# Performance work log

Measured on AMD Instinct MI355X. Metric: run time of the kernel, lower is better.

Reference implementation:

```python
import jax, jax.numpy as jnp
import numpy as np

N_NODES = 50000
N_EDGES = 800000
IN_F = 256
HID = 128
OUT_F = 128
HEADS = 4
NEG_SLOPE = 0.2


def setup_inputs() -> dict:
    key = jax.random.key(0)
    ks = jax.random.split(key, 10)
    x = jax.random.normal(ks[0], (N_NODES, IN_F), dtype=jnp.float32)
    edge_index = jax.random.randint(ks[1], (2, N_EDGES), 0, N_NODES, dtype=jnp.int64)
    # layer 1: in=256 -> heads=4, ch=128
    W1 = jax.random.normal(ks[2], (HEADS * HID, IN_F), dtype=jnp.float32) / np.sqrt(IN_F)
    att_src1 = jax.random.normal(ks[3], (HEADS, HID), dtype=jnp.float32) / np.sqrt(HID)
    att_dst1 = jax.random.normal(ks[4], (HEADS, HID), dtype=jnp.float32) / np.sqrt(HID)
    b1 = jnp.zeros((HID,), dtype=jnp.float32)
    # layer 2: in=128 -> heads=4, ch=128
    W2 = jax.random.normal(ks[5], (HEADS * OUT_F, HID), dtype=jnp.float32) / np.sqrt(HID)
    att_src2 = jax.random.normal(ks[6], (HEADS, OUT_F), dtype=jnp.float32) / np.sqrt(OUT_F)
    att_dst2 = jax.random.normal(ks[7], (HEADS, OUT_F), dtype=jnp.float32) / np.sqrt(OUT_F)
    b2 = jnp.zeros((OUT_F,), dtype=jnp.float32)
    return {"x": x, "edge_index": edge_index,
            "W1": W1, "att_src1": att_src1, "att_dst1": att_dst1, "b1": b1,
            "W2": W2, "att_src2": att_src2, "att_dst2": att_dst2, "b2": b2}


def gat_conv(x, src, dst, W, att_src, att_dst, b, heads, ch):
    n = x.shape[0]
    xh = (x @ W.T).reshape(n, heads, ch)                 # [N,H,C]
    a_s = jnp.einsum('nhc,hc->nh', xh, att_src)          # [N,H]
    a_d = jnp.einsum('nhc,hc->nh', xh, att_dst)
    alpha = a_s[src] + a_d[dst]                          # [E,H]
    alpha = jnp.where(alpha >= 0, alpha, NEG_SLOPE * alpha)
    # segment softmax over destination nodes
    amax = jax.ops.segment_max(alpha, dst, num_segments=n)
    amax = jnp.where(jnp.isfinite(amax), amax, 0.0)
    e = jnp.exp(alpha - amax[dst])                       # [E,H]
    denom = jax.ops.segment_sum(e, dst, num_segments=n)  # [N,H]
    coef = e / (denom[dst] + 1e-16)                      # [E,H]
    msg = xh[src] * coef[:, :, None]                     # [E,H,C]
    out = jax.ops.segment_sum(msg, dst, num_segments=n)  # [N,H,C]
    return out.mean(axis=1) + b                          # concat=False -> mean over heads


def reference(x, edge_index, W1, att_src1, att_dst1, b1, W2, att_src2, att_dst2, b2):
    n = x.shape[0]
    loops = jnp.arange(n, dtype=edge_index.dtype)
    src = jnp.concatenate([edge_index[0], loops])        # add_self_loops=True (PyG default)
    dst = jnp.concatenate([edge_index[1], loops])
    h = gat_conv(x, src, dst, W1, att_src1, att_dst1, b1, HEADS, HID)
    return gat_conv(h, src, dst, W2, att_src2, att_dst2, b2, HEADS, OUT_F)
```

## Files before the change

kernel.cpp:

```cpp
#include <hip/hip_runtime.h>
#include <hip/hip_fp16.h>
#include <math.h>

#define N_NODES 50000
#define MPAD    50176
#define N_EDGES 800000
#define E_TOT   (N_EDGES + N_NODES)
#define EB      ((E_TOT + 255) / 256)
#define HEADS   4
#define NEG_SLOPE 0.2f
#define SBLK    ((N_NODES + 255) / 256)

typedef unsigned int u32;
typedef unsigned short u16;
typedef __attribute__((ext_vector_type(8))) _Float16 f16x8;
typedef __attribute__((ext_vector_type(4))) float f32x4;



__global__ __launch_bounds__(256) void prep(const int* __restrict__ ei,
                                            int* __restrict__ deg,
                                            const float* __restrict__ W1,
                                            __half* __restrict__ B1,
                                            const float* __restrict__ W2,
                                            __half* __restrict__ B2,
                                            const float* __restrict__ att_s1,
                                            const float* __restrict__ att_d1,
                                            const float* __restrict__ att_s2,
                                            const float* __restrict__ att_d2,
                                            float* __restrict__ ws1,
                                            float* __restrict__ wd1,
                                            float* __restrict__ ws2,
                                            float* __restrict__ wd2) {
  int b = blockIdx.x, tid = threadIdx.x;
  if (b < EB) {
    int e = b * 256 + tid;
    if (e < E_TOT) {
      int dst = (e < N_EDGES) ? ei[N_EDGES + e] : (e - N_EDGES);
      atomicAdd(&deg[dst], 1);
    }
    return;
  }
  if (b < EB + 128) {
    int k4 = (b - EB) * 256 + tid;
    float4 v = ((const float4*)W1)[k4];
    __half2 h01 = __float22half2_rn(make_float2(v.x, v.y));
    __half2 h23 = __float22half2_rn(make_float2(v.z, v.w));
    uint2 pk = make_uint2(*(u32*)&h01, *(u32*)&h23);
    int r = k4 >> 6, h = r >> 7, j = r & 127;
    ((uint2*)B1)[j * 256 + h * 64 + (k4 & 63)] = pk;
    return;
  }
  if (b < EB + 192) {
    int k4 = (b - EB - 128) * 256 + tid;
    float4 v = ((const float4*)W2)[k4];
    __half2 h01 = __float22half2_rn(make_float2(v.x, v.y));
    __half2 h23 = __float22half2_rn(make_float2(v.z, v.w));
    uint2 pk = make_uint2(*(u32*)&h01, *(u32*)&h23);
    int r = k4 >> 5, h = r >> 7, j = r & 127;
    ((uint2*)B2)[j * 128 + h * 32 + (k4 & 31)] = pk;
    return;
  }
  int bw = b - (EB + 192);
  int h = bw & 3;
  if (bw < 8) {
    const float* att = (bw < 4) ? att_s1 : att_d1;
    float* o = (bw < 4) ? ws1 : wd1;
    int k = tid;
    float acc = 0.f;
    for (int c = 0; c < 128; ++c)
      acc = fmaf(att[h * 128 + c], W1[(size_t)(h * 128 + c) * 256 + k], acc);
    o[h * 256 + k] = acc;
  } else {
    const float* att = (bw < 12) ? att_s2 : att_d2;
    float* o = (bw < 12) ? ws2 : wd2;
    if (tid < 128) {
      int k = tid;
      float acc = 0.f;
      for (int c = 0; c < 128; ++c)
        acc = fmaf(att[h * 128 + c], W2[(size_t)(h * 128 + c) * 128 + k], acc);
      o[h * 128 + k] = acc;
    }
  }
}


__global__ __launch_bounds__(256) void scan_blocks(const int* __restrict__ deg,
                                                   int* __restrict__ row_ptr,
                                                   int* __restrict__ bsum) {
  __shared__ int sh[256];
  int tid = threadIdx.x;
  int idx = blockIdx.x * 256 + tid;
  int v = (idx < N_NODES) ? deg[idx] : 0;
  sh[tid] = v;
  __syncthreads();
#pragma unroll
  for (int off = 1; off < 256; off <<= 1) {
    int t = (tid >= off) ? sh[tid - off] : 0;
    __syncthreads();
    sh[tid] += t;
    __syncthreads();
  }
  if (idx < N_NODES) row_ptr[idx + 1] = sh[tid];
  if (tid == 255) bsum[blockIdx.x] = sh[255];
}

__global__ __launch_bounds__(256) void scan_tops(int* __restrict__ bsum) {
  __shared__ int sh[256];
  int tid = threadIdx.x;
  int v = (tid < SBLK) ? bsum[tid] : 0;
  sh[tid] = v;
  __syncthreads();
#pragma unroll
  for (int off = 1; off < 256; off <<= 1) {
    int t = (tid >= off) ? sh[tid - off] : 0;
    __syncthreads();
    sh[tid] += t;
    __syncthreads();
  }
  if (tid < SBLK) bsum[tid] = sh[tid] - v;
}

__global__ __launch_bounds__(256) void scan_add(const int* __restrict__ bsum,
                                                int* __restrict__ row_ptr) {
  int idx = blockIdx.x * 256 + threadIdx.x;
  int off = bsum[blockIdx.x];
  if (idx < N_NODES) row_ptr[idx + 1] += off;
  if (idx == 0) row_ptr[0] = 0;
}

__device__ __forceinline__ float leaky_exp(float a) {
  a = (a >= 0.f) ? a : NEG_SLOPE * a;
  return __expf(a);
}

__global__ __launch_bounds__(256) void scatter_edges_w(const int* __restrict__ ei,
                                                       const int* __restrict__ row_ptr,
                                                       int* __restrict__ cursor,
                                                       const float* __restrict__ as_,
                                                       const float* __restrict__ ad_,
                                                       int* __restrict__ col,
                                                       int* __restrict__ dstarr,
                                                       float4* __restrict__ wtab) {
  int e = blockIdx.x * 256 + threadIdx.x;
  if (e >= E_TOT) return;
  int src, dst;
  if (e < N_EDGES) { src = ei[e]; dst = ei[N_EDGES + e]; }
  else             { src = e - N_EDGES; dst = src; }
  int pos = atomicAdd(&cursor[dst], 1);
  int slot = row_ptr[dst] + pos;
  col[slot] = src;
  dstarr[slot] = dst;
  float4 a = ((const float4*)as_)[src];
  float4 d = ((const float4*)ad_)[dst];
  float4 w;
  w.x = leaky_exp(a.x + d.x);
  w.y = leaky_exp(a.y + d.y);
  w.z = leaky_exp(a.z + d.z);
  w.w = leaky_exp(a.w + d.w);
  wtab[slot] = w;
}

__global__ __launch_bounds__(256) void edge_weights2(const int* __restrict__ col,
                                                     const int* __restrict__ dstarr,
                                                     const float* __restrict__ as_,
                                                     const float* __restrict__ ad_,
                                                     float4* __restrict__ wtab) {
  int i = blockIdx.x * 256 + threadIdx.x;
  if (i >= E_TOT) return;
  int src = col[i], dst = dstarr[i];
  float4 a = ((const float4*)as_)[src];
  float4 d = ((const float4*)ad_)[dst];
  float4 w;
  w.x = leaky_exp(a.x + d.x);
  w.y = leaky_exp(a.y + d.y);
  w.z = leaky_exp(a.z + d.z);
  w.w = leaky_exp(a.w + d.w);
  wtab[i] = w;
}


__global__ __launch_bounds__(256) void prep_x(const float* __restrict__ x,
                                              const float* __restrict__ ws1,
                                              const float* __restrict__ wd1,
                                              __half* __restrict__ x16,
                                              float* __restrict__ as_,
                                              float* __restrict__ ad_) {
  int node = (blockIdx.x * 256 + threadIdx.x) >> 6;
  if (node >= N_NODES) return;
  int lane = threadIdx.x & 63;
  int c4 = lane * 4;
  f32x4 xv = *(const f32x4*)(x + (size_t)node * 256 + c4);
  __half2 h01 = __float22half2_rn(make_float2(xv[0], xv[1]));
  __half2 h23 = __float22half2_rn(make_float2(xv[2], xv[3]));
  uint2 pk = make_uint2(*(u32*)&h01, *(u32*)&h23);
  *(uint2*)(x16 + (size_t)node * 256 + c4) = pk;
  float p[8];
#pragma unroll
  for (int v = 0; v < 4; ++v) {
    f32x4 w = *(const f32x4*)(ws1 + v * 256 + c4);
    p[v] = xv[0] * w[0] + xv[1] * w[1] + xv[2] * w[2] + xv[3] * w[3];
    f32x4 u = *(const f32x4*)(wd1 + v * 256 + c4);
    p[4 + v] = xv[0] * u[0] + xv[1] * u[1] + xv[2] * u[2] + xv[3] * u[3];
  }
#pragma unroll
  for (int k = 0; k < 8; ++k)
#pragma unroll
    for (int m = 1; m < 64; m <<= 1)
      p[k] += __shfl_xor(p[k], m, 64);
  if (lane == 0) {
    *(float4*)(as_ + (size_t)node * 4) = make_float4(p[0], p[1], p[2], p[3]);
    *(float4*)(ad_ + (size_t)node * 4) = make_float4(p[4], p[5], p[6], p[7]);
  }
}


__global__ __launch_bounds__(256) void score2(const __half* __restrict__ hrow,
                                              const float* __restrict__ ws2,
                                              const float* __restrict__ wd2,
                                              float* __restrict__ as_,
                                              float* __restrict__ ad_) {
  int node = (blockIdx.x * 256 + threadIdx.x) >> 6;
  if (node >= N_NODES) return;
  int lane = threadIdx.x & 63, c = lane * 2;
  float2 f = __half22float2(*(const __half2*)(hrow + (size_t)node * 128 + c));
  float p[8];
#pragma unroll
  for (int v = 0; v < 4; ++v) {
    float2 w = *(const float2*)(ws2 + v * 128 + c);
    p[v] = f.x * w.x + f.y * w.y;
    float2 u = *(const float2*)(wd2 + v * 128 + c);
    p[4 + v] = f.x * u.x + f.y * u.y;
  }
#pragma unroll
  for (int k = 0; k < 8; ++k)
#pragma unroll
    for (int m = 1; m < 64; m <<= 1)
      p[k] += __shfl_xor(p[k], m, 64);
  if (lane == 0) {
    *(float4*)(as_ + (size_t)node * 4) = make_float4(p[0], p[1], p[2], p[3]);
    *(float4*)(ad_ + (size_t)node * 4) = make_float4(p[4], p[5], p[6], p[7]);
  }
}


template <int CPL>
__global__ __launch_bounds__(256) void gat_aggregate_w(
    const __half* __restrict__ tbl, const float4* __restrict__ wtab,
    const int* __restrict__ row_ptr, const int* __restrict__ col,
    __half* __restrict__ agg) {
  constexpr int CHIN = CPL * 64;
  int node = (blockIdx.x * 256 + threadIdx.x) >> 6;
  if (node >= N_NODES) return;
  int lane = threadIdx.x & 63, cb = lane * CPL;
  const __half* tb = tbl + cb;
  int s = __builtin_amdgcn_readfirstlane(row_ptr[node]);
  int e = __builtin_amdgcn_readfirstlane(row_ptr[node + 1]);

  float acc[4][CPL];
#pragma unroll
  for (int h = 0; h < 4; ++h)
#pragma unroll
    for (int c = 0; c < CPL; ++c) acc[h][c] = 0.f;
  float den[4] = {0.f, 0.f, 0.f, 0.f};

  auto accum = [&](uint2 q, float4 w) {
    float wv[4] = {w.x, w.y, w.z, w.w};
#pragma unroll
    for (int h = 0; h < 4; ++h) den[h] += wv[h];
    float f[CPL];
    float2 f0 = __half22float2(*(__half2*)&q.x);
    f[0] = f0.x; f[1] = f0.y;
    if (CPL == 4) {
      float2 f1 = __half22float2(*(__half2*)&q.y);
      f[2] = f1.x; f[3] = f1.y;
    }
#pragma unroll
    for (int h = 0; h < 4; ++h)
#pragma unroll
      for (int c = 0; c < CPL; ++c)
        acc[h][c] = fmaf(wv[h], f[c], acc[h][c]);
  };
  auto loadq = [&](int src) -> uint2 {
    if (CPL == 4) return *(const uint2*)(tb + (size_t)src * CHIN);
    uint2 r; r.x = *(const u32*)(tb + (size_t)src * CHIN); r.y = 0;
    return r;
  };

  int i = s;
  for (; i + 4 <= e; i += 4) {
    int s0 = __builtin_amdgcn_readfirstlane(col[i]);
    int s1 = __builtin_amdgcn_readfirstlane(col[i + 1]);
    int s2 = __builtin_amdgcn_readfirstlane(col[i + 2]);
    int s3 = __builtin_amdgcn_readfirstlane(col[i + 3]);
    float4 w0 = wtab[i],     w1 = wtab[i + 1];
    float4 w2 = wtab[i + 2], w3 = wtab[i + 3];
    uint2 q0 = loadq(s0), q1 = loadq(s1), q2 = loadq(s2), q3 = loadq(s3);
    accum(q0, w0); accum(q1, w1); accum(q2, w2); accum(q3, w3);
  }
  for (; i < e; ++i) {
    int s0 = __builtin_amdgcn_readfirstlane(col[i]);
    float4 w0 = wtab[i];
    accum(loadq(s0), w0);
  }

#pragma unroll
  for (int h = 0; h < 4; ++h) {
    float inv = 1.f / (den[h] + 1e-16f);
    if (CPL == 4) {
      __half2 o0 = __float22half2_rn(make_float2(acc[h][0] * inv, acc[h][1] * inv));
      __half2 o1 = __float22half2_rn(make_float2(acc[h][2] * inv, acc[h][3] * inv));
      *(uint2*)(agg + (size_t)node * 4 * CHIN + h * CHIN + cb) =
          make_uint2(*(u32*)&o0, *(u32*)&o1);
    } else {
      __half2 o0 = __float22half2_rn(make_float2(acc[h][0] * inv, acc[h][1] * inv));
      *(u32*)(agg + (size_t)node * 4 * CHIN + h * CHIN + cb) = *(u32*)&o0;
    }
  }
}


#define GLD16(gp, lp)                                                          \
  __builtin_amdgcn_global_load_lds(                                            \
      (const __attribute__((address_space(1))) u32*)(gp),                      \
      (__attribute__((address_space(3))) u32*)(lp), 16, 0, 0)

template <int K, bool HALF_OUT>
__global__ __launch_bounds__(512, 4) void gemm_mean(
    const __half* __restrict__ A, const __half* __restrict__ Bm,
    const float* __restrict__ bias, void* __restrict__ outv) {
  __shared__ u16 sA[256 * 32];
  __shared__ u16 sB[128 * 32];
  const int tid = threadIdx.x, lane = tid & 63, wave = tid >> 6;
  const int m0 = blockIdx.x * 256;
  const int wm = (wave >> 1) * 64, wn = (wave & 1) * 64;
  const int t = lane & 15, quad = lane >> 4;

  f32x4 acc[4][4];
#pragma unroll
  for (int i = 0; i < 4; i++)
#pragma unroll
    for (int j = 0; j < 4; j++) acc[i][j] = (f32x4){0.f, 0.f, 0.f, 0.f};

  const char* gpA[2]; u32 offA[2];
#pragma unroll
  for (int r = 0; r < 2; ++r) {
    int c = tid + r * 512;
    int row = c >> 2, w16 = c & 3;
    gpA[r] = (const char*)A + ((size_t)(m0 + row) * K) * 2 + w16 * 16;
    offA[r] = (u32)c * 16;
  }
  const char* gpB;
  {
    int row = tid >> 2, w16 = tid & 3;
    gpB = (const char*)Bm + ((size_t)row * K) * 2 + w16 * 16;
  }
  u32 offB = (u32)tid * 16;

  for (int k0 = 0; k0 < K; k0 += 32) {
    __syncthreads();
#pragma unroll
    for (int r = 0; r < 2; ++r) { GLD16(gpA[r], (char*)sA + offA[r]); gpA[r] += 64; }
    GLD16(gpB, (char*)sB + offB); gpB += 64;
    __syncthreads();

    f16x8 a[4], b[4];
#pragma unroll
    for (int i = 0; i < 4; ++i) {
      a[i] = *(const f16x8*)&sA[(wm + t + i * 16) * 32 + quad * 8];
      b[i] = *(const f16x8*)&sB[(wn + t + i * 16) * 32 + quad * 8];
    }
#pragma unroll
    for (int i = 0; i < 4; ++i)
#pragma unroll
      for (int j = 0; j < 4; ++j)
        acc[i][j] = __builtin_amdgcn_mfma_f32_16x16x32_f16(a[i], b[j], acc[i][j], 0, 0, 0);
  }

  float bv[4];
#pragma unroll
  for (int j = 0; j < 4; ++j) bv[j] = bias[wn + j * 16 + t];
#pragma unroll
  for (int i = 0; i < 4; ++i)
#pragma unroll
    for (int j = 0; j < 4; ++j)
#pragma unroll
      for (int r = 0; r < 4; ++r) {
        int m = m0 + wm + i * 16 + quad * 4 + r;
        if (m < N_NODES) {
          int n = wn + j * 16 + t;
          float v = 0.25f * acc[i][j][r] + bv[j];
          if (HALF_OUT) ((__half*)outv)[(size_t)m * 128 + n] = __float2half(v);
          else          ((float*)outv)[(size_t)m * 128 + n] = v;
        }
      }
}


extern "C" void kernel_launch(void* const* d_in, const int* in_sizes, int n_in,
                              void* d_out, int out_size, void* d_ws, size_t ws_size,
                              hipStream_t stream) {
  const float* x      = (const float*)d_in[0];
  const int*   ei     = (const int*)  d_in[1];
  const float* W1     = (const float*)d_in[2];
  const float* att_s1 = (const float*)d_in[3];
  const float* att_d1 = (const float*)d_in[4];
  const float* b1     = (const float*)d_in[5];
  const float* W2     = (const float*)d_in[6];
  const float* att_s2 = (const float*)d_in[7];
  const float* att_d2 = (const float*)d_in[8];
  const float* b2     = (const float*)d_in[9];
  float* out = (float*)d_out;

  char* ws = (char*)d_ws;
  size_t off = 0;
  auto alloc = [&](size_t bytes) -> void* {
    void* p = ws + off;
    off += (bytes + 255) & ~(size_t)255;
    return p;
  };
  __half* x16  = (__half*)alloc((size_t)MPAD * 256 * 2);
  __half* agg1 = (__half*)alloc((size_t)MPAD * 1024 * 2);
  __half* B1p  = (__half*)alloc((size_t)128 * 1024 * 2);
  __half* B2p  = (__half*)alloc((size_t)128 * 512 * 2);
  float* ws1 = (float*)alloc(4 * 256 * 4);
  float* wd1 = (float*)alloc(4 * 256 * 4);
  float* ws2 = (float*)alloc(4 * 128 * 4);
  float* wd2 = (float*)alloc(4 * 128 * 4);
  float* as1 = (float*)alloc((size_t)N_NODES * 4 * 4);
  float* ad1 = (float*)alloc((size_t)N_NODES * 4 * 4);
  float* as2 = (float*)alloc((size_t)N_NODES * 4 * 4);
  float* ad2 = (float*)alloc((size_t)N_NODES * 4 * 4);
  int*   row_ptr = (int*)alloc((size_t)(N_NODES + 1) * 4);
  int*   deg     = (int*)alloc((size_t)N_NODES * 4);
  int*   cursor  = (int*)alloc((size_t)N_NODES * 4);
  int*   bsum    = (int*)alloc((size_t)256 * 4);
  int*   col     = (int*)alloc((size_t)E_TOT * 4);
  int*   dstarr  = (int*)alloc((size_t)E_TOT * 4);
  float4* wtab   = (float4*)alloc((size_t)E_TOT * 16);

  __half* out1 = x16;
  __half* agg2 = agg1;

  const int edge_blocks = (E_TOT + 255) / 256;
  const int node_wave_blocks = (N_NODES + 3) / 4;

  hipMemsetAsync(deg, 0, (size_t)N_NODES * 2 * 4 + 256, stream);
  prep<<<EB + 208, 256, 0, stream>>>(ei, deg, W1, B1p, W2, B2p,
                                     att_s1, att_d1, att_s2, att_d2,
                                     ws1, wd1, ws2, wd2);
  scan_blocks<<<SBLK, 256, 0, stream>>>(deg, row_ptr, bsum);
  scan_tops<<<1, 256, 0, stream>>>(bsum);
  scan_add<<<SBLK, 256, 0, stream>>>(bsum, row_ptr);

  prep_x<<<node_wave_blocks, 256, 0, stream>>>(x, ws1, wd1, x16, as1, ad1);
  scatter_edges_w<<<edge_blocks, 256, 0, stream>>>(ei, row_ptr, cursor,
                                                   as1, ad1, col, dstarr, wtab);
  gat_aggregate_w<4><<<node_wave_blocks, 256, 0, stream>>>(
      x16, wtab, row_ptr, col, agg1);
  gemm_mean<1024, true><<<MPAD / 256, 512, 0, stream>>>(agg1, B1p, b1, out1);

  score2<<<node_wave_blocks, 256, 0, stream>>>(out1, ws2, wd2, as2, ad2);
  edge_weights2<<<edge_blocks, 256, 0, stream>>>(col, dstarr, as2, ad2, wtab);
  gat_aggregate_w<2><<<node_wave_blocks, 256, 0, stream>>>(
      out1, wtab, row_ptr, col, agg2);
  gemm_mean<512, false><<<MPAD / 256, 512, 0, stream>>>(agg2, B2p, b2, out);
}
```

Measured before the change: 440.1 us.

## Record edge slot positions during degree count and pack src/dst pairs

The degree-counting atomic now stores each edge's returned position, so the CSR scatter no longer needs a second cursor atomic pass. Source and destination are packed into one int2 array, replacing separate col and dst arrays, and a single edge_weights kernel serves both layers. The layer-1 edge-weight computation now runs as its own kernel reading the packed array, which adds a launch and an extra pass over the edges. The aggregate kernels read source indices at stride 2 from the packed array, which halves the useful bytes per cache line.

```diff
diff --git a/kernel.cpp b/kernel.cpp
--- a/kernel.cpp
+++ b/kernel.cpp
@@ -20,6 +20,7 @@
 
 __global__ __launch_bounds__(256) void prep(const int* __restrict__ ei,
                                             int* __restrict__ deg,
+                                            int* __restrict__ epos,
                                             const float* __restrict__ W1,
                                             __half* __restrict__ B1,
                                             const float* __restrict__ W2,
@@ -37,7 +38,7 @@
     int e = b * 256 + tid;
     if (e < E_TOT) {
       int dst = (e < N_EDGES) ? ei[N_EDGES + e] : (e - N_EDGES);
-      atomicAdd(&deg[dst], 1);
+      epos[e] = atomicAdd(&deg[dst], 1);
     }
     return;
   }
@@ -134,43 +135,30 @@
   return __expf(a);
 }
 
-__global__ __launch_bounds__(256) void scatter_edges_w(const int* __restrict__ ei,
-                                                       const int* __restrict__ row_ptr,
-                                                       int* __restrict__ cursor,
-                                                       const float* __restrict__ as_,
-                                                       const float* __restrict__ ad_,
-                                                       int* __restrict__ col,
-                                                       int* __restrict__ dstarr,
-                                                       float4* __restrict__ wtab) {
+
+__global__ __launch_bounds__(256) void scatter_pos(const int* __restrict__ ei,
+                                                   const int* __restrict__ epos,
+                                                   const int* __restrict__ row_ptr,
+                                                   int2* __restrict__ col2) {
   int e = blockIdx.x * 256 + threadIdx.x;
   if (e >= E_TOT) return;
   int src, dst;
   if (e < N_EDGES) { src = ei[e]; dst = ei[N_EDGES + e]; }
   else             { src = e - N_EDGES; dst = src; }
-  int pos = atomicAdd(&cursor[dst], 1);
-  int slot = row_ptr[dst] + pos;
-  col[slot] = src;
-  dstarr[slot] = dst;
-  float4 a = ((const float4*)as_)[src];
-  float4 d = ((const float4*)ad_)[dst];
-  float4 w;
-  w.x = leaky_exp(a.x + d.x);
-  w.y = leaky_exp(a.y + d.y);
-  w.z = leaky_exp(a.z + d.z);
-  w.w = leaky_exp(a.w + d.w);
-  wtab[slot] = w;
-}
-
-__global__ __launch_bounds__(256) void edge_weights2(const int* __restrict__ col,
-                                                     const int* __restrict__ dstarr,
-                                                     const float* __restrict__ as_,
-                                                     const float* __restrict__ ad_,
-                                                     float4* __restrict__ wtab) {
+  int slot = row_ptr[dst] + epos[e];
+  col2[slot] = make_int2(src, dst);
+}
+
+
+__global__ __launch_bounds__(256) void edge_weights(const int2* __restrict__ col2,
+                                                    const float* __restrict__ as_,
+                                                    const float* __restrict__ ad_,
+                                                    float4* __restrict__ wtab) {
   int i = blockIdx.x * 256 + threadIdx.x;
   if (i >= E_TOT) return;
-  int src = col[i], dst = dstarr[i];
-  float4 a = ((const float4*)as_)[src];
-  float4 d = ((const float4*)ad_)[dst];
+  int2 sd = col2[i];
+  float4 a = ((const float4*)as_)[sd.x];
+  float4 d = ((const float4*)ad_)[sd.y];
   float4 w;
   w.x = leaky_exp(a.x + d.x);
   w.y = leaky_exp(a.y + d.y);
@@ -247,9 +235,10 @@
 template <int CPL>
 __global__ __launch_bounds__(256) void gat_aggregate_w(
     const __half* __restrict__ tbl, const float4* __restrict__ wtab,
-    const int* __restrict__ row_ptr, const int* __restrict__ col,
+    const int* __restrict__ row_ptr, const int2* __restrict__ col2,
     __half* __restrict__ agg) {
   constexpr int CHIN = CPL * 64;
+  const int* colx = (const int*)col2;
   int node = (blockIdx.x * 256 + threadIdx.x) >> 6;
   if (node >= N_NODES) return;
   int lane = threadIdx.x & 63, cb = lane * CPL;
@@ -289,17 +278,17 @@
 
   int i = s;
   for (; i + 4 <= e; i += 4) {
-    int s0 = __builtin_amdgcn_readfirstlane(col[i]);
-    int s1 = __builtin_amdgcn_readfirstlane(col[i + 1]);
-    int s2 = __builtin_amdgcn_readfirstlane(col[i + 2]);
-    int s3 = __builtin_amdgcn_readfirstlane(col[i + 3]);
+    int s0 = __builtin_amdgcn_readfirstlane(colx[2 * i]);
+    int s1 = __builtin_amdgcn_readfirstlane(colx[2 * i + 2]);
+    int s2 = __builtin_amdgcn_readfirstlane(colx[2 * i + 4]);
+    int s3 = __builtin_amdgcn_readfirstlane(colx[2 * i + 6]);
     float4 w0 = wtab[i],     w1 = wtab[i + 1];
     float4 w2 = wtab[i + 2], w3 = wtab[i + 3];
     uint2 q0 = loadq(s0), q1 = loadq(s1), q2 = loadq(s2), q3 = loadq(s3);
     accum(q0, w0); accum(q1, w1); accum(q2, w2); accum(q3, w3);
   }
   for (; i < e; ++i) {
-    int s0 = __builtin_amdgcn_readfirstlane(col[i]);
+    int s0 = __builtin_amdgcn_readfirstlane(colx[2 * i]);
     float4 w0 = wtab[i];
     accum(loadq(s0), w0);
   }
@@ -433,10 +422,9 @@
   float* ad2 = (float*)alloc((size_t)N_NODES * 4 * 4);
   int*   row_ptr = (int*)alloc((size_t)(N_NODES + 1) * 4);
   int*   deg     = (int*)alloc((size_t)N_NODES * 4);
-  int*   cursor  = (int*)alloc((size_t)N_NODES * 4);
   int*   bsum    = (int*)alloc((size_t)256 * 4);
-  int*   col     = (int*)alloc((size_t)E_TOT * 4);
-  int*   dstarr  = (int*)alloc((size_t)E_TOT * 4);
+  int*   epos    = (int*)alloc((size_t)E_TOT * 4);
+  int2*  col2    = (int2*)alloc((size_t)E_TOT * 8);
   float4* wtab   = (float4*)alloc((size_t)E_TOT * 16);
 
   __half* out1 = x16;
@@ -445,24 +433,24 @@
   const int edge_blocks = (E_TOT + 255) / 256;
   const int node_wave_blocks = (N_NODES + 3) / 4;
 
-  hipMemsetAsync(deg, 0, (size_t)N_NODES * 2 * 4 + 256, stream);
-  prep<<<EB + 208, 256, 0, stream>>>(ei, deg, W1, B1p, W2, B2p,
+  hipMemsetAsync(deg, 0, (size_t)N_NODES * 4, stream);
+  prep<<<EB + 208, 256, 0, stream>>>(ei, deg, epos, W1, B1p, W2, B2p,
                                      att_s1, att_d1, att_s2, att_d2,
                                      ws1, wd1, ws2, wd2);
   scan_blocks<<<SBLK, 256, 0, stream>>>(deg, row_ptr, bsum);
   scan_tops<<<1, 256, 0, stream>>>(bsum);
   scan_add<<<SBLK, 256, 0, stream>>>(bsum, row_ptr);
+  scatter_pos<<<edge_blocks, 256, 0, stream>>>(ei, epos, row_ptr, col2);
 
   prep_x<<<node_wave_blocks, 256, 0, stream>>>(x, ws1, wd1, x16, as1, ad1);
-  scatter_edges_w<<<edge_blocks, 256, 0, stream>>>(ei, row_ptr, cursor,
-                                                   as1, ad1, col, dstarr, wtab);
+  edge_weights<<<edge_blocks, 256, 0, stream>>>(col2, as1, ad1, wtab);
   gat_aggregate_w<4><<<node_wave_blocks, 256, 0, stream>>>(
-      x16, wtab, row_ptr, col, agg1);
+      x16, wtab, row_ptr, col2, agg1);
   gemm_mean<1024, true><<<MPAD / 256, 512, 0, stream>>>(agg1, B1p, b1, out1);
 
   score2<<<node_wave_blocks, 256, 0, stream>>>(out1, ws2, wd2, as2, ad2);
-  edge_weights2<<<edge_blocks, 256, 0, stream>>>(col, dstarr, as2, ad2, wtab);
+  edge_weights<<<edge_blocks, 256, 0, stream>>>(col2, as2, ad2, wtab);
   gat_aggregate_w<2><<<node_wave_blocks, 256, 0, stream>>>(
-      out1, wtab, row_ptr, col, agg2);
+      out1, wtab, row_ptr, col2, agg2);
   gemm_mean<512, false><<<MPAD / 256, 512, 0, stream>>>(agg2, B2p, b2, out);
 }
```

New measurement: 406.6 us. -7.6%, faster.
